# Optimization experiments

Hardware: AMD Instinct MI355X
Metric: run time of the kernel (lower is better)

## Reference

```python
import jax, jax.numpy as jnp
import numpy as np

nC, STEP, ROW = 28, 2, 256
COL = ROW + (nC - 1) * STEP  # 310

# 1/alpha normalization for A_pinv: count of overlapping shifted channels per column
_counts = np.zeros((COL,), np.float32)
for _i in range(nC):
    _counts[_i * STEP:_i * STEP + ROW] += 1.0
ALPHA = jnp.asarray(1.0 / _counts)  # [COL]


def conv1x1(x, w, b):
    # x: [B,C,H,W], w: [O,C], b: [O]
    return jnp.einsum('bchw,oc->bohw', x, w) + b[None, :, None, None]


def dwconv5(x, w, b):
    # depthwise 5x5, SAME padding; w: [C,1,5,5]
    out = jax.lax.conv_general_dilated(
        x, w, window_strides=(1, 1), padding='SAME',
        dimension_numbers=('NCHW', 'OIHW', 'NCHW'),
        feature_group_count=x.shape[1])
    return out + b[None, :, None, None]


def mask_guided(m, w1, b1, w2, b2, dw, db):
    m1 = conv1x1(m, w1, b1)
    attn = jax.nn.sigmoid(dwconv5(conv1x1(m1, w2, b2), dw, db))
    emb = m1 * attn + m1
    return jnp.where(emb == 0, jnp.asarray(1e-6, emb.dtype), emb)


def A_op(x, M):
    # shift-and-add: [B,28,256,256] -> [B,1,256,310]
    z = x * M
    y = jnp.zeros((x.shape[0], 1, ROW, COL), x.dtype)
    for i in range(nC):
        y = y.at[:, :, :, i * STEP:i * STEP + ROW].add(z[:, i:i + 1])
    return y


def A_pinv_op(y, M):
    # normalize then extract shifted windows: [B,1,256,310] -> [B,28,256,256]
    z = y * ALPHA  # broadcast over last dim
    x = jnp.stack([z[:, 0, :, i * STEP:i * STEP + ROW] for i in range(nC)], axis=1)
    return x * M


def setup_inputs() -> dict:
    key = jax.random.key(0)
    ks = jax.random.split(key, 16)
    B = 16
    inp = {
        'y': jax.random.normal(ks[0], (B, 1, ROW, COL), jnp.float32),
        'Phi': jax.random.uniform(ks[1], (B, nC, ROW, ROW), jnp.float32),
        'x_pre': jax.random.normal(ks[2], (B, nC, ROW, ROW), jnp.float32),
        'delta': jnp.asarray([0.1], jnp.float32),
        'mm_w1': jax.random.normal(ks[3], (nC, nC), jnp.float32) * 0.1,
        'mm_b1': jax.random.normal(ks[4], (nC,), jnp.float32) * 0.1,
        'mm_w2': jax.random.normal(ks[5], (nC, nC), jnp.float32) * 0.1,
        'mm_b2': jax.random.normal(ks[6], (nC,), jnp.float32) * 0.1,
        'mm_dw': jax.random.normal(ks[7], (nC, 1, 5, 5), jnp.float32) * 0.1,
        'mm_db': jax.random.normal(ks[8], (nC,), jnp.float32) * 0.1,
        'pv_w1': jax.random.normal(ks[9], (nC, nC), jnp.float32) * 0.1,
        'pv_b1': jax.random.normal(ks[10], (nC,), jnp.float32) * 0.1,
        'pv_w2': jax.random.normal(ks[11], (nC, nC), jnp.float32) * 0.1,
        'pv_b2': jax.random.normal(ks[12], (nC,), jnp.float32) * 0.1,
        'pv_dw': jax.random.normal(ks[13], (nC, 1, 5, 5), jnp.float32) * 0.1,
        'pv_db': jax.random.normal(ks[14], (nC,), jnp.float32) * 0.1,
    }
    return inp


def reference(y, Phi, x_pre, delta,
              mm_w1, mm_b1, mm_w2, mm_b2, mm_dw, mm_db,
              pv_w1, pv_b1, pv_w2, pv_b2, pv_dw, pv_db):
    Phi_learned = mask_guided(Phi, mm_w1, mm_b1, mm_w2, mm_b2, mm_dw, mm_db)
    temp = y - A_op(x_pre, Phi_learned)
    Phi_pinv_learned = mask_guided(Phi, pv_w1, pv_b1, pv_w2, pv_b2, pv_dw, pv_db)
    x_init = x_pre + delta * A_pinv_op(temp, Phi_pinv_learned)
    return x_init
```

## Files before the change

### kernel.cpp

```cpp
#include <hip/hip_runtime.h>
#include <hip/hip_bf16.h>
#include <cstdint>

#define NC 28
#define HW 65536
#define ROWW 256
#define COLW 310
#define BATCH 16

typedef __hip_bfloat16 bf16;

__device__ __forceinline__ unsigned int pkh(float lo, float hi) {
    auto h = __builtin_amdgcn_cvt_pkrtz(lo, hi);
    return __builtin_bit_cast(unsigned int, h);
}
__device__ __forceinline__ float h2f_lo(unsigned int u) {
    return (float)__builtin_bit_cast(_Float16, (unsigned short)(u & 0xffffu));
}
__device__ __forceinline__ float h2f_hi(unsigned int u) {
    return (float)__builtin_bit_cast(_Float16, (unsigned short)(u >> 16));
}
__device__ __forceinline__ void pkfma16(unsigned int& acc, unsigned int w, unsigned int x) {
    asm("v_pk_fma_f16 %0, %1, %2, %0" : "+v"(acc) : "s"(w), "v"(x));
}
__device__ __forceinline__ void gl_f32x2(float2& d, const float* p) {
    asm volatile("global_load_dwordx2 %0, %1, off" : "=v"(d) : "v"(p));
}
__device__ __forceinline__ void gl_b32(unsigned int& d, const unsigned short* p) {
    asm volatile("global_load_dword %0, %1, off" : "=v"(d) : "v"(p));
}
__device__ __forceinline__ void wait_vm0() {
    asm volatile("s_waitcnt vmcnt(0)" ::: "memory");
    __builtin_amdgcn_sched_barrier(0);
}

#define REP28A(X) X(0) X(1) X(2) X(3) X(4) X(5) X(6) X(7) X(8) X(9) X(10) X(11) X(12) X(13) \
                  X(14) X(15) X(16) X(17) X(18) X(19) X(20) X(21) X(22) X(23) X(24) X(25) X(26) X(27)

#define HDR_BYTES 16384

__global__ void k0_prep(const float* __restrict__ w1mm, const float* __restrict__ w1pv,
                        const float* __restrict__ w2mm, const float* __restrict__ w2pv,
                        const float* __restrict__ b1mm, const float* __restrict__ b1pv,
                        const float* __restrict__ b2mm, const float* __restrict__ b2pv,
                        const float* __restrict__ dwm,  const float* __restrict__ dwp,
                        const float* __restrict__ dbm,  const float* __restrict__ dbp,
                        unsigned int* __restrict__ hdr)
{
    int t = threadIdx.x;
    for (int e = t; e < 784; e += 256) {
        int c = e / 28, o = e - c * 28;
        hdr[e]       = pkh(w1mm[o * 28 + c], w1pv[o * 28 + c]);
        hdr[784 + e] = pkh(w2mm[e], w2pv[e]);
    }
    if (t < 28) {
        hdr[1568 + t] = pkh(b1mm[t], b1pv[t]);
        hdr[1596 + t] = pkh(b2mm[t], b2pv[t]);
        hdr[2324 + t] = pkh(dbm[t], dbp[t]);
    }
    for (int e = t; e < 700; e += 256)
        hdr[1624 + e] = pkh(dwm[e], dwp[e]);
    float* alpha = (float*)(hdr + 2352);
    for (int col = t; col < COLW; col += 256) {
        int imin = (col > 255) ? ((col - 254) >> 1) : 0;
        int imax = min(27, col >> 1);
        alpha[col] = 1.0f / (float)(imax - imin + 1);
    }
}

__global__ __launch_bounds__(256, 3) void k1_conv1x1(
    const float* __restrict__ Phi, const unsigned int* __restrict__ hdr,
    unsigned int* __restrict__ t_pk, unsigned int* __restrict__ m1_pk)
{
    int idx = blockIdx.x * 256 + threadIdx.x;
    int b   = idx >> 14;
    int hw4 = (idx & 16383) << 2;
    const float* phi = Phi + (size_t)b * NC * HW + hw4;
    const unsigned int* w1h = hdr;
    const unsigned int* w2h = hdr + 784;
    const unsigned int* b1h = hdr + 1568;
    const unsigned int* b2h = hdr + 1596;

#define DECL_M(i) unsigned int MA##i = b1h[i], MB##i = MA##i, MC##i = MA##i, MD##i = MA##i;
    REP28A(DECL_M)
#undef DECL_M

    float4 PQ0, PQ1, PQ2, PQ3, PQ4;
#define GLX4(D, C) asm volatile("global_load_dwordx4 %0, %1, off" : "=v"(D) : "v"(phi + (size_t)(C) * HW))
#define VMW(N) do { asm volatile("s_waitcnt vmcnt(" #N ")" ::: "memory"); \
                    __builtin_amdgcn_sched_barrier(0); } while(0)
#define FMA_M(i) pkfma16(MA##i, wr1_[i], pa); pkfma16(MB##i, wr1_[i], pb); \
                 pkfma16(MC##i, wr1_[i], pc); pkfma16(MD##i, wr1_[i], pd);
#define K1CONS(C, S) do { \
    unsigned int pa = pkh(PQ##S.x, PQ##S.x); \
    unsigned int pb = pkh(PQ##S.y, PQ##S.y); \
    unsigned int pc = pkh(PQ##S.z, PQ##S.z); \
    unsigned int pd = pkh(PQ##S.w, PQ##S.w); \
    const unsigned int* wr1_ = w1h + (C) * NC; \
    REP28A(FMA_M) \
} while(0)

    GLX4(PQ0, 0); GLX4(PQ1, 1); GLX4(PQ2, 2); GLX4(PQ3, 3);
    GLX4(PQ4, 4);  VMW(4); K1CONS(0, 0);
    GLX4(PQ0, 5);  VMW(4); K1CONS(1, 1);
    GLX4(PQ1, 6);  VMW(4); K1CONS(2, 2);
    GLX4(PQ2, 7);  VMW(4); K1CONS(3, 3);
    GLX4(PQ3, 8);  VMW(4); K1CONS(4, 4);
    GLX4(PQ4, 9);  VMW(4); K1CONS(5, 0);
    GLX4(PQ0, 10); VMW(4); K1CONS(6, 1);
    GLX4(PQ1, 11); VMW(4); K1CONS(7, 2);
    GLX4(PQ2, 12); VMW(4); K1CONS(8, 3);
    GLX4(PQ3, 13); VMW(4); K1CONS(9, 4);
    GLX4(PQ4, 14); VMW(4); K1CONS(10, 0);
    GLX4(PQ0, 15); VMW(4); K1CONS(11, 1);
    GLX4(PQ1, 16); VMW(4); K1CONS(12, 2);
    GLX4(PQ2, 17); VMW(4); K1CONS(13, 3);
    GLX4(PQ3, 18); VMW(4); K1CONS(14, 4);
    GLX4(PQ4, 19); VMW(4); K1CONS(15, 0);
    GLX4(PQ0, 20); VMW(4); K1CONS(16, 1);
    GLX4(PQ1, 21); VMW(4); K1CONS(17, 2);
    GLX4(PQ2, 22); VMW(4); K1CONS(18, 3);
    GLX4(PQ3, 23); VMW(4); K1CONS(19, 4);
    GLX4(PQ4, 24); VMW(4); K1CONS(20, 0);
    GLX4(PQ0, 25); VMW(4); K1CONS(21, 1);
    GLX4(PQ1, 26); VMW(4); K1CONS(22, 2);
    GLX4(PQ2, 27); VMW(4); K1CONS(23, 3);
    VMW(3); K1CONS(24, 4);
    VMW(2); K1CONS(25, 0);
    VMW(1); K1CONS(26, 1);
    VMW(0); K1CONS(27, 2);
#undef K1CONS
#undef FMA_M
#undef VMW
#undef GLX4

    size_t base = (size_t)b * NC * HW + hw4;
#define ST_M(i) *reinterpret_cast<uint4*>(m1_pk + base + (size_t)(i) * HW) = \
    make_uint4(MA##i, MB##i, MC##i, MD##i);
    REP28A(ST_M)
#undef ST_M

    for (int o = 0; o < NC; o++) {
        const unsigned int* wr2_ = w2h + o * NC;
        unsigned int Ta = b2h[o], Tb = Ta, Tc = Ta, Td = Ta;
#define FMA_T(i) pkfma16(Ta, wr2_[i], MA##i); pkfma16(Tb, wr2_[i], MB##i); \
                 pkfma16(Tc, wr2_[i], MC##i); pkfma16(Td, wr2_[i], MD##i);
        REP28A(FMA_T)
#undef FMA_T
        *reinterpret_cast<uint4*>(t_pk + base + (size_t)o * HW) = make_uint4(Ta, Tb, Tc, Td);
    }
}

#define TR 16
#define LROW 264

#define LDROW(S, LR) do { \
    const uint2* rp_ = reinterpret_cast<const uint2*>(&st[(LR) * LROW + 2 + cc]); \
    uint2 a_ = rp_[0], b_ = rp_[1], c_ = rp_[2]; \
    W##S##0 = a_.x; W##S##1 = a_.y; W##S##2 = b_.x; \
    W##S##3 = b_.y; W##S##4 = c_.x; W##S##5 = c_.y; \
} while(0)

#define PRE(S, R) do { \
    size_t o_ = cbase + (size_t)(h0 + (R)) * 256 + cc; \
    mu##S = *reinterpret_cast<const uint2*>(m1_pk + o_); \
} while(0)

#define TAPR(S, B) \
    pkfma16(acc0, wq[(B)+0], W##S##0); pkfma16(acc1, wq[(B)+0], W##S##1); \
    pkfma16(acc0, wq[(B)+1], W##S##1); pkfma16(acc1, wq[(B)+1], W##S##2); \
    pkfma16(acc0, wq[(B)+2], W##S##2); pkfma16(acc1, wq[(B)+2], W##S##3); \
    pkfma16(acc0, wq[(B)+3], W##S##3); pkfma16(acc1, wq[(B)+3], W##S##4); \
    pkfma16(acc0, wq[(B)+4], W##S##4); pkfma16(acc1, wq[(B)+4], W##S##5);

#define CROW2(R, PS, S0,S1,S2,S3,S4) do { \
    unsigned int acc0 = dbc, acc1 = dbc; \
    TAPR(S0, 0) TAPR(S1, 5) TAPR(S2, 10) TAPR(S3, 15) TAPR(S4, 20) \
    float am0 = h2f_lo(acc0), ap0 = h2f_hi(acc0); \
    float am1 = h2f_lo(acc1), ap1 = h2f_hi(acc1); \
    float atm0 = __builtin_amdgcn_rcpf(1.f + __expf(-am0)); \
    float atp0 = __builtin_amdgcn_rcpf(1.f + __expf(-ap0)); \
    float atm1 = __builtin_amdgcn_rcpf(1.f + __expf(-am1)); \
    float atp1 = __builtin_amdgcn_rcpf(1.f + __expf(-ap1)); \
    float m1m0 = h2f_lo(mu##PS.x), m1p0 = h2f_hi(mu##PS.x); \
    float m1m1 = h2f_lo(mu##PS.y), m1p1 = h2f_hi(mu##PS.y); \
    float em0 = fmaf(m1m0, atm0, m1m0); \
    float ep0 = fmaf(m1p0, atp0, m1p0); \
    float em1 = fmaf(m1m1, atm1, m1m1); \
    float ep1 = fmaf(m1p1, atp1, m1p1); \
    if (em0 == 0.f) em0 = 1e-6f; \
    if (ep0 == 0.f) ep0 = 1e-6f; \
    if (em1 == 0.f) em1 = 1e-6f; \
    if (ep1 == 0.f) ep1 = 1e-6f; \
    size_t off_ = cbase + (size_t)(h0 + (R)) * 256 + cc; \
    *reinterpret_cast<unsigned int*>(phm + off_) = pkh(em0, em1); \
    *reinterpret_cast<unsigned int*>(php + off_) = pkh(ep0, ep1); \
} while(0)

__global__ __launch_bounds__(256, 4) void k2_attn(
    const unsigned int* __restrict__ t_pk, const unsigned int* __restrict__ m1_pk,
    const unsigned int* __restrict__ hdr,
    unsigned short* __restrict__ phm, unsigned short* __restrict__ php)
{
    __shared__ unsigned int st[(TR + 4) * LROW];

    int bid = blockIdx.x;
    int rt = bid & 15;
    int c  = (bid >> 4) % NC;
    int b  = (bid >> 4) / NC;
    int r0 = rt * TR;
    size_t cbase = ((size_t)b * NC + c) * HW;
    int tid = threadIdx.x;
    int lane = tid & 63;
    int wv = tid >> 6;
    int cc = (tid & 127) * 2;
    int half = tid >> 7;
    int lbase = half * 8;
    int h0 = r0 + lbase;

    if (tid < 80) {
        int rr = tid >> 2, jj = tid & 3;
        st[rr * LROW + ((jj < 2) ? 2 + jj : 258 + jj)] = 0u;
    }

#pragma unroll
    for (int j = 0; j < 5; j++) {
        int r = wv * 5 + j;
        int gr = r0 - 2 + r;
        if (gr >= 0 && gr < 256) {
            const unsigned int* gsrc = t_pk + cbase + (size_t)gr * 256 + lane * 4;
            __builtin_amdgcn_global_load_lds(
                (const __attribute__((address_space(1))) unsigned int*)gsrc,
                (__attribute__((address_space(3))) unsigned int*)&st[r * LROW + 4],
                16, 0, 0);
        } else {
            st[r * LROW + 4 + lane]       = 0u;
            st[r * LROW + 4 + 64 + lane]  = 0u;
            st[r * LROW + 4 + 128 + lane] = 0u;
            st[r * LROW + 4 + 192 + lane] = 0u;
        }
    }

    unsigned int wq[25];
#pragma unroll
    for (int k = 0; k < 25; k++)
        wq[k] = __builtin_amdgcn_readfirstlane(hdr[1624 + c * 25 + k]);
    unsigned int dbc = __builtin_amdgcn_readfirstlane(hdr[2324 + c]);

    uint2 mu0, mu1, mu2, mu3, mu4;
    PRE(0, 0); PRE(1, 1); PRE(2, 2); PRE(3, 3);

    __syncthreads();

    unsigned int W00,W01,W02,W03,W04,W05, W10,W11,W12,W13,W14,W15,
                 W20,W21,W22,W23,W24,W25, W30,W31,W32,W33,W34,W35,
                 W40,W41,W42,W43,W44,W45;

    LDROW(0, lbase + 0); LDROW(1, lbase + 1); LDROW(2, lbase + 2); LDROW(3, lbase + 3);
    LDROW(4, lbase + 4);  PRE(4, 4);  CROW2(0, 0, 0,1,2,3,4);
    LDROW(0, lbase + 5);  PRE(0, 5);  CROW2(1, 1, 1,2,3,4,0);
    LDROW(1, lbase + 6);  PRE(1, 6);  CROW2(2, 2, 2,3,4,0,1);
    LDROW(2, lbase + 7);  PRE(2, 7);  CROW2(3, 3, 3,4,0,1,2);
    LDROW(3, lbase + 8);              CROW2(4, 4, 4,0,1,2,3);
    LDROW(4, lbase + 9);              CROW2(5, 0, 0,1,2,3,4);
    LDROW(0, lbase + 10);             CROW2(6, 1, 1,2,3,4,0);
    LDROW(1, lbase + 11);             CROW2(7, 2, 2,3,4,0,1);
}

__global__ __launch_bounds__(256, 8) void k34_out(
    const float* __restrict__ y, const float* __restrict__ x_pre,
    const unsigned short* __restrict__ phm, const unsigned short* __restrict__ php,
    const unsigned int* __restrict__ hdr, const float* __restrict__ delta,
    float* __restrict__ out)
{
    __shared__ float temp[312];

    int tid = threadIdx.x;
    int b = blockIdx.x >> 8;
    int h = blockIdx.x & 255;
    const float* alpha = (const float*)(hdr + 2352);
    size_t rowbase = ((size_t)b * NC) * HW + (size_t)h * 256;
    const float* yr = y + ((size_t)b * 256 + h) * COLW;

    if (tid < 155) {
        int c0 = tid * 2;
        float2 yv = *reinterpret_cast<const float2*>(yr + c0);
        float acc0 = yv.x, acc1 = yv.y;
        float2 xs0,xs1,xs2,xs3,xs4,xs5,xs6;
        unsigned int es0,es1,es2,es3,es4,es5,es6;

#define ISSUE(J, I) do { \
        int cs_ = c0 - 2 * (I); \
        bool v_ = ((unsigned)cs_) < 256u; \
        size_t off_ = rowbase + (size_t)(I) * HW + (v_ ? cs_ : 0); \
        gl_f32x2(xs##J, x_pre + off_); \
        gl_b32(es##J, phm + off_); \
    } while(0)
#define CONSUME(J, I) do { \
        int cs_ = c0 - 2 * (I); \
        bool v_ = ((unsigned)cs_) < 256u; \
        acc0 -= v_ ? xs##J.x * h2f_lo(es##J) : 0.f; \
        acc1 -= v_ ? xs##J.y * h2f_hi(es##J) : 0.f; \
    } while(0)
#define GRP(B0) \
        ISSUE(0,(B0)+0); ISSUE(1,(B0)+1); ISSUE(2,(B0)+2); ISSUE(3,(B0)+3); \
        ISSUE(4,(B0)+4); ISSUE(5,(B0)+5); ISSUE(6,(B0)+6); \
        wait_vm0(); \
        CONSUME(0,(B0)+0); CONSUME(1,(B0)+1); CONSUME(2,(B0)+2); CONSUME(3,(B0)+3); \
        CONSUME(4,(B0)+4); CONSUME(5,(B0)+5); CONSUME(6,(B0)+6);

        GRP(0) GRP(7) GRP(14) GRP(21)
#undef GRP
#undef CONSUME
#undef ISSUE

        float2 av = *reinterpret_cast<const float2*>(alpha + c0);
        *reinterpret_cast<float2*>(&temp[c0]) = make_float2(acc0 * av.x, acc1 * av.y);
    }
    __syncthreads();

    float d = delta[0];
    int wp = (tid & 127) * 2;
    int ihalf = tid >> 7;
#pragma unroll
    for (int g = 0; g < 2; g++) {
        int i0 = ihalf * 14 + g * 7;
        float2 xp0,xp1,xp2,xp3,xp4,xp5,xp6;
        unsigned int ep0,ep1,ep2,ep3,ep4,ep5,ep6;
#define ISSUE2(J) do { \
        size_t off_ = rowbase + (size_t)(i0 + (J)) * HW + wp; \
        gl_f32x2(xp##J, x_pre + off_); \
        gl_b32(ep##J, php + off_); \
    } while(0)
#define STORE2(J) do { \
        int i_ = i0 + (J); \
        size_t off_ = rowbase + (size_t)i_ * HW + wp; \
        float2 tv = *reinterpret_cast<const float2*>(&temp[wp + 2 * i_]); \
        float2 o2; \
        o2.x = fmaf(d * tv.x, h2f_lo(ep##J), xp##J.x); \
        o2.y = fmaf(d * tv.y, h2f_hi(ep##J), xp##J.y); \
        *reinterpret_cast<float2*>(out + off_) = o2; \
    } while(0)
        ISSUE2(0); ISSUE2(1); ISSUE2(2); ISSUE2(3); ISSUE2(4); ISSUE2(5); ISSUE2(6);
        wait_vm0();
        STORE2(0); STORE2(1); STORE2(2); STORE2(3); STORE2(4); STORE2(5); STORE2(6);
#undef ISSUE2
#undef STORE2
    }
}

extern "C" void kernel_launch(void* const* d_in, const int* in_sizes, int n_in,
                              void* d_out, int out_size, void* d_ws, size_t ws_size,
                              hipStream_t stream)
{
    const float* y     = (const float*)d_in[0];
    const float* Phi   = (const float*)d_in[1];
    const float* x_pre = (const float*)d_in[2];
    const float* delta = (const float*)d_in[3];
    const float* mm_w1 = (const float*)d_in[4];
    const float* mm_b1 = (const float*)d_in[5];
    const float* mm_w2 = (const float*)d_in[6];
    const float* mm_b2 = (const float*)d_in[7];
    const float* mm_dw = (const float*)d_in[8];
    const float* mm_db = (const float*)d_in[9];
    const float* pv_w1 = (const float*)d_in[10];
    const float* pv_b1 = (const float*)d_in[11];
    const float* pv_w2 = (const float*)d_in[12];
    const float* pv_b2 = (const float*)d_in[13];
    const float* pv_dw = (const float*)d_in[14];
    const float* pv_db = (const float*)d_in[15];
    float* out = (float*)d_out;

    char* ws = (char*)d_ws;
    const size_t A = (size_t)BATCH * NC * HW * 4;
    unsigned int*   hdr   = (unsigned int*)ws;
    unsigned int*   t_pk  = (unsigned int*)(ws + HDR_BYTES);
    unsigned int*   m1_pk = (unsigned int*)(ws + HDR_BYTES + A);
    unsigned short* phm   = (unsigned short*)(ws + HDR_BYTES + 2 * A);
    unsigned short* php   = (unsigned short*)(ws + HDR_BYTES + 2 * A + A / 2);

    k0_prep<<<1, 256, 0, stream>>>(mm_w1, pv_w1, mm_w2, pv_w2,
                                   mm_b1, pv_b1, mm_b2, pv_b2,
                                   mm_dw, pv_dw, mm_db, pv_db, hdr);
    k1_conv1x1<<<1024, 256, 0, stream>>>(Phi, hdr, t_pk, m1_pk);
    k2_attn<<<BATCH * NC * 16, 256, 0, stream>>>(t_pk, m1_pk, hdr, phm, php);
    k34_out<<<BATCH * 256, 256, 0, stream>>>(y, x_pre, phm, php, hdr, delta, out);
}
```

Before: 228.9 us.

## Cache x_pre row in LDS for output pass; use native half2 FMA vectors

The output kernel now stores the x_pre values it loads during the residual pass into a 28x256 shared-memory tile and reads them back from there in the final pass, instead of reloading x_pre from global memory. Separately, the inline-asm packed f16 FMAs are replaced with native _Float16 vector arithmetic so the compiler can schedule them. The LDS tile is about 28 KB per block, so the launch bound drops from 8 to 5 blocks per SM, trading occupancy for less global traffic.

```diff
diff --git a/kernel.cpp b/kernel.cpp
--- a/kernel.cpp
+++ b/kernel.cpp
@@ -9,19 +9,19 @@
 #define BATCH 16
 
 typedef __hip_bfloat16 bf16;
+typedef _Float16 h2v __attribute__((ext_vector_type(2)));
 
 __device__ __forceinline__ unsigned int pkh(float lo, float hi) {
     auto h = __builtin_amdgcn_cvt_pkrtz(lo, hi);
     return __builtin_bit_cast(unsigned int, h);
 }
+__device__ __forceinline__ h2v u2h(unsigned int u) { return __builtin_bit_cast(h2v, u); }
+__device__ __forceinline__ unsigned int h2u(h2v h) { return __builtin_bit_cast(unsigned int, h); }
 __device__ __forceinline__ float h2f_lo(unsigned int u) {
     return (float)__builtin_bit_cast(_Float16, (unsigned short)(u & 0xffffu));
 }
 __device__ __forceinline__ float h2f_hi(unsigned int u) {
     return (float)__builtin_bit_cast(_Float16, (unsigned short)(u >> 16));
-}
-__device__ __forceinline__ void pkfma16(unsigned int& acc, unsigned int w, unsigned int x) {
-    asm("v_pk_fma_f16 %0, %1, %2, %0" : "+v"(acc) : "s"(w), "v"(x));
 }
 __device__ __forceinline__ void gl_f32x2(float2& d, const float* p) {
     asm volatile("global_load_dwordx2 %0, %1, off" : "=v"(d) : "v"(p));
@@ -81,7 +81,7 @@
     const unsigned int* b1h = hdr + 1568;
     const unsigned int* b2h = hdr + 1596;
 
-#define DECL_M(i) unsigned int MA##i = b1h[i], MB##i = MA##i, MC##i = MA##i, MD##i = MA##i;
+#define DECL_M(i) h2v MA##i = u2h(b1h[i]), MB##i = MA##i, MC##i = MA##i, MD##i = MA##i;
     REP28A(DECL_M)
 #undef DECL_M
 
@@ -89,14 +89,14 @@
 #define GLX4(D, C) asm volatile("global_load_dwordx4 %0, %1, off" : "=v"(D) : "v"(phi + (size_t)(C) * HW))
 #define VMW(N) do { asm volatile("s_waitcnt vmcnt(" #N ")" ::: "memory"); \
                     __builtin_amdgcn_sched_barrier(0); } while(0)
-#define FMA_M(i) pkfma16(MA##i, wr1_[i], pa); pkfma16(MB##i, wr1_[i], pb); \
-                 pkfma16(MC##i, wr1_[i], pc); pkfma16(MD##i, wr1_[i], pd);
+#define FMA_M(i) MA##i = wr1_[i] * pa + MA##i; MB##i = wr1_[i] * pb + MB##i; \
+                 MC##i = wr1_[i] * pc + MC##i; MD##i = wr1_[i] * pd + MD##i;
 #define K1CONS(C, S) do { \
-    unsigned int pa = pkh(PQ##S.x, PQ##S.x); \
-    unsigned int pb = pkh(PQ##S.y, PQ##S.y); \
-    unsigned int pc = pkh(PQ##S.z, PQ##S.z); \
-    unsigned int pd = pkh(PQ##S.w, PQ##S.w); \
-    const unsigned int* wr1_ = w1h + (C) * NC; \
+    h2v pa = u2h(pkh(PQ##S.x, PQ##S.x)); \
+    h2v pb = u2h(pkh(PQ##S.y, PQ##S.y)); \
+    h2v pc = u2h(pkh(PQ##S.z, PQ##S.z)); \
+    h2v pd = u2h(pkh(PQ##S.w, PQ##S.w)); \
+    const h2v* wr1_ = (const h2v*)(w1h + (C) * NC); \
     REP28A(FMA_M) \
 } while(0)
 
@@ -136,18 +136,19 @@
 
     size_t base = (size_t)b * NC * HW + hw4;
 #define ST_M(i) *reinterpret_cast<uint4*>(m1_pk + base + (size_t)(i) * HW) = \
-    make_uint4(MA##i, MB##i, MC##i, MD##i);
+    make_uint4(h2u(MA##i), h2u(MB##i), h2u(MC##i), h2u(MD##i));
     REP28A(ST_M)
 #undef ST_M
 
     for (int o = 0; o < NC; o++) {
-        const unsigned int* wr2_ = w2h + o * NC;
-        unsigned int Ta = b2h[o], Tb = Ta, Tc = Ta, Td = Ta;
-#define FMA_T(i) pkfma16(Ta, wr2_[i], MA##i); pkfma16(Tb, wr2_[i], MB##i); \
-                 pkfma16(Tc, wr2_[i], MC##i); pkfma16(Td, wr2_[i], MD##i);
+        const h2v* wr2_ = (const h2v*)(w2h + o * NC);
+        h2v Ta = u2h(b2h[o]), Tb = Ta, Tc = Ta, Td = Ta;
+#define FMA_T(i) Ta = wr2_[i] * MA##i + Ta; Tb = wr2_[i] * MB##i + Tb; \
+                 Tc = wr2_[i] * MC##i + Tc; Td = wr2_[i] * MD##i + Td;
         REP28A(FMA_T)
 #undef FMA_T
-        *reinterpret_cast<uint4*>(t_pk + base + (size_t)o * HW) = make_uint4(Ta, Tb, Tc, Td);
+        *reinterpret_cast<uint4*>(t_pk + base + (size_t)o * HW) =
+            make_uint4(h2u(Ta), h2u(Tb), h2u(Tc), h2u(Td));
     }
 }
 
@@ -157,8 +158,8 @@
 #define LDROW(S, LR) do { \
     const uint2* rp_ = reinterpret_cast<const uint2*>(&st[(LR) * LROW + 2 + cc]); \
     uint2 a_ = rp_[0], b_ = rp_[1], c_ = rp_[2]; \
-    W##S##0 = a_.x; W##S##1 = a_.y; W##S##2 = b_.x; \
-    W##S##3 = b_.y; W##S##4 = c_.x; W##S##5 = c_.y; \
+    W##S##0 = u2h(a_.x); W##S##1 = u2h(a_.y); W##S##2 = u2h(b_.x); \
+    W##S##3 = u2h(b_.y); W##S##4 = u2h(c_.x); W##S##5 = u2h(c_.y); \
 } while(0)
 
 #define PRE(S, R) do { \
@@ -167,17 +168,17 @@
 } while(0)
 
 #define TAPR(S, B) \
-    pkfma16(acc0, wq[(B)+0], W##S##0); pkfma16(acc1, wq[(B)+0], W##S##1); \
-    pkfma16(acc0, wq[(B)+1], W##S##1); pkfma16(acc1, wq[(B)+1], W##S##2); \
-    pkfma16(acc0, wq[(B)+2], W##S##2); pkfma16(acc1, wq[(B)+2], W##S##3); \
-    pkfma16(acc0, wq[(B)+3], W##S##3); pkfma16(acc1, wq[(B)+3], W##S##4); \
-    pkfma16(acc0, wq[(B)+4], W##S##4); pkfma16(acc1, wq[(B)+4], W##S##5);
+    acc0 = wqh[(B)+0] * W##S##0 + acc0; acc1 = wqh[(B)+0] * W##S##1 + acc1; \
+    acc0 = wqh[(B)+1] * W##S##1 + acc0; acc1 = wqh[(B)+1] * W##S##2 + acc1; \
+    acc0 = wqh[(B)+2] * W##S##2 + acc0; acc1 = wqh[(B)+2] * W##S##3 + acc1; \
+    acc0 = wqh[(B)+3] * W##S##3 + acc0; acc1 = wqh[(B)+3] * W##S##4 + acc1; \
+    acc0 = wqh[(B)+4] * W##S##4 + acc0; acc1 = wqh[(B)+4] * W##S##5 + acc1;
 
 #define CROW2(R, PS, S0,S1,S2,S3,S4) do { \
-    unsigned int acc0 = dbc, acc1 = dbc; \
+    h2v acc0 = dbch, acc1 = dbch; \
     TAPR(S0, 0) TAPR(S1, 5) TAPR(S2, 10) TAPR(S3, 15) TAPR(S4, 20) \
-    float am0 = h2f_lo(acc0), ap0 = h2f_hi(acc0); \
-    float am1 = h2f_lo(acc1), ap1 = h2f_hi(acc1); \
+    float am0 = (float)acc0.x, ap0 = (float)acc0.y; \
+    float am1 = (float)acc1.x, ap1 = (float)acc1.y; \
     float atm0 = __builtin_amdgcn_rcpf(1.f + __expf(-am0)); \
     float atp0 = __builtin_amdgcn_rcpf(1.f + __expf(-ap0)); \
     float atm1 = __builtin_amdgcn_rcpf(1.f + __expf(-am1)); \
@@ -241,20 +242,20 @@
         }
     }
 
-    unsigned int wq[25];
+    h2v wqh[25];
 #pragma unroll
     for (int k = 0; k < 25; k++)
-        wq[k] = __builtin_amdgcn_readfirstlane(hdr[1624 + c * 25 + k]);
-    unsigned int dbc = __builtin_amdgcn_readfirstlane(hdr[2324 + c]);
+        wqh[k] = u2h(__builtin_amdgcn_readfirstlane(hdr[1624 + c * 25 + k]));
+    h2v dbch = u2h(__builtin_amdgcn_readfirstlane(hdr[2324 + c]));
 
     uint2 mu0, mu1, mu2, mu3, mu4;
     PRE(0, 0); PRE(1, 1); PRE(2, 2); PRE(3, 3);
 
     __syncthreads();
 
-    unsigned int W00,W01,W02,W03,W04,W05, W10,W11,W12,W13,W14,W15,
-                 W20,W21,W22,W23,W24,W25, W30,W31,W32,W33,W34,W35,
-                 W40,W41,W42,W43,W44,W45;
+    h2v W00,W01,W02,W03,W04,W05, W10,W11,W12,W13,W14,W15,
+        W20,W21,W22,W23,W24,W25, W30,W31,W32,W33,W34,W35,
+        W40,W41,W42,W43,W44,W45;
 
     LDROW(0, lbase + 0); LDROW(1, lbase + 1); LDROW(2, lbase + 2); LDROW(3, lbase + 3);
     LDROW(4, lbase + 4);  PRE(4, 4);  CROW2(0, 0, 0,1,2,3,4);
@@ -267,13 +268,14 @@
     LDROW(1, lbase + 11);             CROW2(7, 2, 2,3,4,0,1);
 }
 
-__global__ __launch_bounds__(256, 8) void k34_out(
+__global__ __launch_bounds__(256, 5) void k34_out(
     const float* __restrict__ y, const float* __restrict__ x_pre,
     const unsigned short* __restrict__ phm, const unsigned short* __restrict__ php,
     const unsigned int* __restrict__ hdr, const float* __restrict__ delta,
     float* __restrict__ out)
 {
     __shared__ float temp[312];
+    __shared__ float xls[NC][256];
 
     int tid = threadIdx.x;
     int b = blockIdx.x >> 8;
@@ -299,6 +301,7 @@
 #define CONSUME(J, I) do { \
         int cs_ = c0 - 2 * (I); \
         bool v_ = ((unsigned)cs_) < 256u; \
+        if (v_) *reinterpret_cast<float2*>(&xls[(I)][cs_]) = xs##J; \
         acc0 -= v_ ? xs##J.x * h2f_lo(es##J) : 0.f; \
         acc1 -= v_ ? xs##J.y * h2f_hi(es##J) : 0.f; \
     } while(0)
@@ -325,20 +328,16 @@
 #pragma unroll
     for (int g = 0; g < 2; g++) {
         int i0 = ihalf * 14 + g * 7;
-        float2 xp0,xp1,xp2,xp3,xp4,xp5,xp6;
         unsigned int ep0,ep1,ep2,ep3,ep4,ep5,ep6;
-#define ISSUE2(J) do { \
-        size_t off_ = rowbase + (size_t)(i0 + (J)) * HW + wp; \
-        gl_f32x2(xp##J, x_pre + off_); \
-        gl_b32(ep##J, php + off_); \
-    } while(0)
+#define ISSUE2(J) gl_b32(ep##J, php + rowbase + (size_t)(i0 + (J)) * HW + wp)
 #define STORE2(J) do { \
         int i_ = i0 + (J); \
         size_t off_ = rowbase + (size_t)i_ * HW + wp; \
         float2 tv = *reinterpret_cast<const float2*>(&temp[wp + 2 * i_]); \
+        float2 xv = *reinterpret_cast<const float2*>(&xls[i_][wp]); \
         float2 o2; \
-        o2.x = fmaf(d * tv.x, h2f_lo(ep##J), xp##J.x); \
-        o2.y = fmaf(d * tv.y, h2f_hi(ep##J), xp##J.y); \
+        o2.x = fmaf(d * tv.x, h2f_lo(ep##J), xv.x); \
+        o2.y = fmaf(d * tv.y, h2f_hi(ep##J), xv.y); \
         *reinterpret_cast<float2*>(out + off_) = o2; \
     } while(0)
         ISSUE2(0); ISSUE2(1); ISSUE2(2); ISSUE2(3); ISSUE2(4); ISSUE2(5); ISSUE2(6);
```

Result: no change. 226.9 us (-0.9%).
